# Kernel tuning notes

Measured on AMD Instinct MI355X. Metric: run time of the kernel, lower is better.

The kernel has to match this reference:

```python
import jax, jax.numpy as jnp
import numpy as np

H = 32  # hidden size


def _gru_layer(x_seq, W_ih, W_hh, b_ih, b_hh):
    """x_seq: [B, T, in] -> outputs [B, T, H], final h [B, H]. PyTorch gate order (r, z, n)."""
    B = x_seq.shape[0]
    # Precompute input projections for all timesteps: [T, B, 3H]
    xw = jnp.einsum('bti,gi->tbg', x_seq, W_ih) + b_ih
    h0 = jnp.zeros((B, H), dtype=x_seq.dtype)

    def step(h, xw_t):
        gh = h @ W_hh.T + b_hh                       # [B, 3H]
        r = jax.nn.sigmoid(xw_t[:, :H] + gh[:, :H])
        z = jax.nn.sigmoid(xw_t[:, H:2 * H] + gh[:, H:2 * H])
        n = jnp.tanh(xw_t[:, 2 * H:] + r * gh[:, 2 * H:])
        h_new = (1.0 - z) * n + z * h
        return h_new, h_new

    h_last, ys = jax.lax.scan(step, h0, xw)
    return jnp.transpose(ys, (1, 0, 2)), h_last       # [B, T, H], [B, H]


def setup_inputs() -> dict:
    key = jax.random.key(0)
    ks = jax.random.split(key, 11)
    s = 1.0 / np.sqrt(H)  # PyTorch GRU init scale
    return {
        'x': jax.random.normal(ks[0], (4096, 512, 32), dtype=jnp.float32),
        'W_ih0': jax.random.uniform(ks[1], (96, 32), jnp.float32, -s, s),
        'W_hh0': jax.random.uniform(ks[2], (96, 32), jnp.float32, -s, s),
        'b_ih0': jax.random.uniform(ks[3], (96,), jnp.float32, -s, s),
        'b_hh0': jax.random.uniform(ks[4], (96,), jnp.float32, -s, s),
        'W_ih1': jax.random.uniform(ks[5], (96, 32), jnp.float32, -s, s),
        'W_hh1': jax.random.uniform(ks[6], (96, 32), jnp.float32, -s, s),
        'b_ih1': jax.random.uniform(ks[7], (96,), jnp.float32, -s, s),
        'b_hh1': jax.random.uniform(ks[8], (96,), jnp.float32, -s, s),
        'W_proj': jax.random.uniform(ks[9], (16, 32), jnp.float32, -s, s),
        'b_proj': jax.random.uniform(ks[10], (16,), jnp.float32, -s, s),
    }


def reference(x, W_ih0, W_hh0, b_ih0, b_hh0, W_ih1, W_hh1, b_ih1, b_hh1, W_proj, b_proj):
    y0, _ = _gru_layer(x, W_ih0, W_hh0, b_ih0, b_hh0)        # layer 0 full sequence
    _, h_last = _gru_layer(y0, W_ih1, W_hh1, b_ih1, b_hh1)   # layer 1 final hidden
    # dropout is identity in eval mode
    return h_last @ W_proj.T + b_proj                        # [B, 16]
```

## Files before the change

### kernel.cpp

```cpp
#include <hip/hip_runtime.h>

using bf16x8 = __attribute__((ext_vector_type(8))) short;
using short8 = __attribute__((ext_vector_type(8))) short;
using s16x4  = __attribute__((ext_vector_type(4))) short;
using f32x4  = __attribute__((ext_vector_type(4))) float;
using u32x4  = __attribute__((ext_vector_type(4))) unsigned;
using ull    = unsigned long long;

#define T_SEQ 512
#define MFMA(A, B, C) __builtin_amdgcn_mfma_f32_16x16x32_bf16((A), (B), (C), 0, 0, 0)

#define BARRIER()                                            \
    do {                                                     \
        __builtin_amdgcn_sched_barrier(0);                   \
        asm volatile("s_waitcnt lgkmcnt(0)" ::: "memory");   \
        __builtin_amdgcn_s_barrier();                        \
        __builtin_amdgcn_sched_barrier(0);                   \
    } while (0)

static constexpr float NL2E  = -1.44269504f;
static constexpr float N2L2E = -2.88539008f;

__device__ __forceinline__ void split8_tr(f32x4 a, f32x4 b, bf16x8& hi, bf16x8& lo) {
    u32x4 ua = __builtin_bit_cast(u32x4, a);
    u32x4 ub = __builtin_bit_cast(u32x4, b);
    u32x4 m  = {0xffff0000u, 0xffff0000u, 0xffff0000u, 0xffff0000u};
    f32x4 ra = a - __builtin_bit_cast(f32x4, ua & m);
    f32x4 rb = b - __builtin_bit_cast(f32x4, ub & m);
    short8 sa  = __builtin_bit_cast(short8, a);
    short8 sb  = __builtin_bit_cast(short8, b);
    short8 sra = __builtin_bit_cast(short8, ra);
    short8 srb = __builtin_bit_cast(short8, rb);
    hi = __builtin_shufflevector(sa, sb, 1, 3, 5, 7, 9, 11, 13, 15);
    lo = __builtin_shufflevector(sra, srb, 1, 3, 5, 7, 9, 11, 13, 15);
}

__device__ __forceinline__ void split4_tr(f32x4 a, s16x4& hi, s16x4& lo) {
    u32x4 ua = __builtin_bit_cast(u32x4, a);
    u32x4 m  = {0xffff0000u, 0xffff0000u, 0xffff0000u, 0xffff0000u};
    f32x4 ra = a - __builtin_bit_cast(f32x4, ua & m);
    short8 sa  = __builtin_bit_cast(short8, a);
    short8 sra = __builtin_bit_cast(short8, ra);
    hi = __builtin_shufflevector(sa, sa, 1, 3, 5, 7);
    lo = __builtin_shufflevector(sra, sra, 1, 3, 5, 7);
}

__device__ __forceinline__ bf16x8 combine8(ull lo8, ull hi8) {
    u32x4 v = {(unsigned)lo8, (unsigned)(lo8 >> 32),
               (unsigned)hi8, (unsigned)(hi8 >> 32)};
    return __builtin_bit_cast(bf16x8, v);
}
__device__ __forceinline__ bf16x8 combine8_sel(ull own, ull other, int m) {
    return combine8(m ? other : own, m ? own : other);
}

__device__ __forceinline__ void mfma9(const bf16x8 (&WH)[3], const bf16x8 (&WL)[3],
                                      bf16x8 inh, bf16x8 inl,
                                      f32x4 c0, f32x4 c1, f32x4 c2,
                                      f32x4& a0, f32x4& a1, f32x4& a2) {
    a0 = MFMA(WH[0], inh, c0); a1 = MFMA(WH[1], inh, c1); a2 = MFMA(WH[2], inh, c2);
    a0 = MFMA(WH[0], inl, a0); a1 = MFMA(WH[1], inl, a1); a2 = MFMA(WH[2], inl, a2);
    a0 = MFMA(WL[0], inh, a0); a1 = MFMA(WL[1], inh, a1); a2 = MFMA(WL[2], inh, a2);
}

__device__ __forceinline__ void gate4(f32x4 aR, f32x4 aZ, f32x4 iN, f32x4 sN,
                                      float (&hf)[4]) {
    float er[4], ez[4];
    #pragma unroll
    for (int j = 0; j < 4; ++j) er[j] = __builtin_amdgcn_exp2f(aR[j] * NL2E);
    #pragma unroll
    for (int j = 0; j < 4; ++j) ez[j] = __builtin_amdgcn_exp2f(aZ[j] * NL2E);
    float gr[4], gz[4];
    #pragma unroll
    for (int j = 0; j < 4; ++j) gr[j] = __builtin_amdgcn_rcpf(1.f + er[j]);
    #pragma unroll
    for (int j = 0; j < 4; ++j) gz[j] = __builtin_amdgcn_rcpf(1.f + ez[j]);
    float en[4];
    #pragma unroll
    for (int j = 0; j < 4; ++j) {
        float u = fmaf(gr[j], sN[j], iN[j]);
        en[j] = __builtin_amdgcn_exp2f(fminf(u * N2L2E, 126.f));
    }
    float qn[4];
    #pragma unroll
    for (int j = 0; j < 4; ++j) qn[j] = __builtin_amdgcn_rcpf(1.f + en[j]);
    #pragma unroll
    for (int j = 0; j < 4; ++j) {
        float nn = fmaf(en[j] * qn[j], -2.f, 1.f);
        hf[j] = fmaf(gz[j], hf[j] - nn, nn);
    }
}

__global__ __launch_bounds__(256, 1)
void gru2_quad(const float* __restrict__ x,
               const float* __restrict__ W_ih0, const float* __restrict__ W_hh0,
               const float* __restrict__ b_ih0, const float* __restrict__ b_hh0,
               const float* __restrict__ W_ih1, const float* __restrict__ W_hh1,
               const float* __restrict__ b_ih1, const float* __restrict__ b_hh1,
               const float* __restrict__ W_proj, const float* __restrict__ b_proj,
               float* __restrict__ out)
{
    const int tid  = threadIdx.x;
    const int wid  = tid >> 6;
    const int L    = wid >> 1;
    const int m    = wid & 1;
    const int lane = tid & 63;
    const int r16  = lane & 15;
    const int q    = lane >> 4;
    const int b0   = blockIdx.x * 16;

    __shared__ ull pubH_[2][2][2][64];
    __shared__ ull pubL_[2][2][2][64];

    const float* Wx = L ? W_ih1 : W_ih0;
    const float* Wh = L ? W_hh1 : W_hh0;
    const float* bx = L ? b_ih1 : b_ih0;
    const float* bh = L ? b_hh1 : b_hh0;

    bf16x8 WxH[3], WxL[3], WhH[3], WhL[3];
    f32x4 bxf[3], bhf[3];
    #pragma unroll
    for (int g = 0; g < 3; ++g) {
        const int tile = 2 * g + m;
        const float* p1 = Wx + (16 * tile + r16) * 32 + 4 * q;
        split8_tr(*(const f32x4*)p1, *(const f32x4*)(p1 + 16), WxH[g], WxL[g]);
        const float* p2 = Wh + (16 * tile + r16) * 32 + 4 * q;
        split8_tr(*(const f32x4*)p2, *(const f32x4*)(p2 + 16), WhH[g], WhL[g]);
        bxf[g] = *(const f32x4*)(bx + 16 * tile + 4 * q);
        bhf[g] = *(const f32x4*)(bh + 16 * tile + 4 * q);
    }

    float hf[4] = {0.f, 0.f, 0.f, 0.f};
    ull ownH = 0, ownL = 0;
    const float* xp = x + (size_t)(b0 + r16) * (T_SEQ * 32) + 4 * q;
    f32x4 xA = {}, xB = {};
    bf16x8 xh_cur = {}, xl_cur = {};

    if (L == 0) {
        f32x4 x0A = *(const f32x4*)(xp);
        f32x4 x0B = *(const f32x4*)(xp + 16);
        xA = *(const f32x4*)(xp + 32);
        xB = *(const f32x4*)(xp + 48);
        split8_tr(x0A, x0B, xh_cur, xl_cur);
        f32x4 iR, iZ, iN;
        mfma9(WxH, WxL, xh_cur, xl_cur, bxf[0], bxf[1], bxf[2], iR, iZ, iN);
        gate4(iR + bhf[0], iZ + bhf[1], iN, bhf[2], hf);
        s16x4 hi4, lo4;
        split4_tr(f32x4{hf[0], hf[1], hf[2], hf[3]}, hi4, lo4);
        ownH = __builtin_bit_cast(ull, hi4);
        ownL = __builtin_bit_cast(ull, lo4);
        pubH_[m][0][0][lane] = ownH;
        pubL_[m][0][0][lane] = ownL;
        split8_tr(xA, xB, xh_cur, xl_cur);
        xA = *(const f32x4*)(xp + 64);
        xB = *(const f32x4*)(xp + 80);
    } else {
        pubH_[m][1][1][lane] = 0;
        pubL_[m][1][1][lane] = 0;
    }

    #pragma unroll 1
    for (int t = 1; t < T_SEQ; ++t) {
        BARRIER();
        const int pPrev = (t - 1) & 1;
        const int pCur  = t & 1;
        f32x4 iR, iZ, iN, sR, sZ, sN;
        if (L == 0) {
            ull oH = pubH_[1 - m][0][pPrev][lane];
            ull oL = pubL_[1 - m][0][pPrev][lane];
            mfma9(WxH, WxL, xh_cur, xl_cur, bxf[0], bxf[1], bxf[2], iR, iZ, iN);
            bf16x8 Sh = combine8_sel(ownH, oH, m);
            bf16x8 Sl = combine8_sel(ownL, oL, m);
            mfma9(WhH, WhL, Sh, Sl, bhf[0], bhf[1], bhf[2], sR, sZ, sN);
            split8_tr(xA, xB, xh_cur, xl_cur);
            const int tn = (t + 2 < T_SEQ) ? t + 2 : T_SEQ - 1;
            xA = *(const f32x4*)(xp + (size_t)tn * 32);
            xB = *(const f32x4*)(xp + (size_t)tn * 32 + 16);
        } else {
            ull i0H = pubH_[0][0][pPrev][lane];
            ull i1H = pubH_[1][0][pPrev][lane];
            ull i0L = pubL_[0][0][pPrev][lane];
            ull i1L = pubL_[1][0][pPrev][lane];
            ull oH  = pubH_[1 - m][1][pCur][lane];
            ull oL  = pubL_[1 - m][1][pCur][lane];
            bf16x8 inh = combine8(i0H, i1H);
            bf16x8 inl = combine8(i0L, i1L);
            mfma9(WxH, WxL, inh, inl, bxf[0], bxf[1], bxf[2], iR, iZ, iN);
            bf16x8 Sh = combine8_sel(ownH, oH, m);
            bf16x8 Sl = combine8_sel(ownL, oL, m);
            mfma9(WhH, WhL, Sh, Sl, bhf[0], bhf[1], bhf[2], sR, sZ, sN);
        }

        gate4(sR + iR, sZ + iZ, iN, sN, hf);

        s16x4 hi4, lo4;
        split4_tr(f32x4{hf[0], hf[1], hf[2], hf[3]}, hi4, lo4);
        ownH = __builtin_bit_cast(ull, hi4);
        ownL = __builtin_bit_cast(ull, lo4);
        const int pW = (L == 0) ? pCur : pPrev;
        pubH_[m][L][pW][lane] = ownH;
        pubL_[m][L][pW][lane] = ownL;
    }

    __syncthreads();
    if (L == 1) {
        bf16x8 inh = combine8(pubH_[0][0][1][lane], pubH_[1][0][1][lane]);
        bf16x8 inl = combine8(pubL_[0][0][1][lane], pubL_[1][0][1][lane]);
        bf16x8 Sh  = combine8_sel(ownH, pubH_[1 - m][1][0][lane], m);
        bf16x8 Sl  = combine8_sel(ownL, pubL_[1 - m][1][0][lane], m);
        f32x4 iR, iZ, iN, sR, sZ, sN;
        mfma9(WxH, WxL, inh, inl, bxf[0], bxf[1], bxf[2], iR, iZ, iN);
        mfma9(WhH, WhL, Sh, Sl, bhf[0], bhf[1], bhf[2], sR, sZ, sN);
        gate4(sR + iR, sZ + iZ, iN, sN, hf);
        s16x4 hi4, lo4;
        split4_tr(f32x4{hf[0], hf[1], hf[2], hf[3]}, hi4, lo4);
        pubH_[m][1][1][lane] = __builtin_bit_cast(ull, hi4);
        pubL_[m][1][1][lane] = __builtin_bit_cast(ull, lo4);
    }
    __syncthreads();

    if (wid == 2) {
        bf16x8 Hh = combine8(pubH_[0][1][1][lane], pubH_[1][1][1][lane]);
        bf16x8 Hl = combine8(pubL_[0][1][1][lane], pubL_[1][1][1][lane]);
        const float* pp = W_proj + r16 * 32 + 4 * q;
        bf16x8 Wph, Wpl;
        split8_tr(*(const f32x4*)pp, *(const f32x4*)(pp + 16), Wph, Wpl);
        f32x4 accp = *(const f32x4*)(b_proj + 4 * q);
        accp = MFMA(Wph, Hh, accp);
        accp = MFMA(Wph, Hl, accp);
        accp = MFMA(Wpl, Hh, accp);
        #pragma unroll
        for (int rg = 0; rg < 4; ++rg)
            out[(b0 + r16) * 16 + 4 * q + rg] = accp[rg];
    }
}

extern "C" void kernel_launch(void* const* d_in, const int* in_sizes, int n_in,
                              void* d_out, int out_size, void* d_ws, size_t ws_size,
                              hipStream_t stream) {
    const float* x      = (const float*)d_in[0];
    const float* W_ih0  = (const float*)d_in[1];
    const float* W_hh0  = (const float*)d_in[2];
    const float* b_ih0  = (const float*)d_in[3];
    const float* b_hh0  = (const float*)d_in[4];
    const float* W_ih1  = (const float*)d_in[5];
    const float* W_hh1  = (const float*)d_in[6];
    const float* b_ih1  = (const float*)d_in[7];
    const float* b_hh1  = (const float*)d_in[8];
    const float* W_proj = (const float*)d_in[9];
    const float* b_proj = (const float*)d_in[10];
    float* out = (float*)d_out;

    const int nb   = in_sizes[0] / (T_SEQ * 32);
    const int grid = nb / 16;

    hipLaunchKernelGGL(gru2_quad, dim3(grid), dim3(256), 0, stream,
                       x, W_ih0, W_hh0, b_ih0, b_hh0,
                       W_ih1, W_hh1, b_ih1, b_hh1, W_proj, b_proj, out);
}
```

Before: 295.6 us.

## Process two 16-row batch groups per block to interleave independent recurrences

Each block now handles 32 batch rows as two independent 16-row groups. The MFMA, gate and LDS exchange work for both groups is interleaved inside each timestep. The aim is to hide the serial latency of the recurrence behind the independent group and to halve the number of barriers per batch row. The cost is half as many blocks, which may leave CUs idle, and longer per-step critical paths.

```diff
diff --git a/kernel.cpp b/kernel.cpp
--- a/kernel.cpp
+++ b/kernel.cpp
@@ -63,42 +63,57 @@
     a0 = MFMA(WL[0], inh, a0); a1 = MFMA(WL[1], inh, a1); a2 = MFMA(WL[2], inh, a2);
 }
 
-__device__ __forceinline__ void gate4(f32x4 aR, f32x4 aZ, f32x4 iN, f32x4 sN,
-                                      float (&hf)[4]) {
-    float er[4], ez[4];
-    #pragma unroll
-    for (int j = 0; j < 4; ++j) er[j] = __builtin_amdgcn_exp2f(aR[j] * NL2E);
-    #pragma unroll
-    for (int j = 0; j < 4; ++j) ez[j] = __builtin_amdgcn_exp2f(aZ[j] * NL2E);
-    float gr[4], gz[4];
-    #pragma unroll
-    for (int j = 0; j < 4; ++j) gr[j] = __builtin_amdgcn_rcpf(1.f + er[j]);
-    #pragma unroll
-    for (int j = 0; j < 4; ++j) gz[j] = __builtin_amdgcn_rcpf(1.f + ez[j]);
-    float en[4];
-    #pragma unroll
-    for (int j = 0; j < 4; ++j) {
-        float u = fmaf(gr[j], sN[j], iN[j]);
-        en[j] = __builtin_amdgcn_exp2f(fminf(u * N2L2E, 126.f));
-    }
-    float qn[4];
-    #pragma unroll
-    for (int j = 0; j < 4; ++j) qn[j] = __builtin_amdgcn_rcpf(1.f + en[j]);
-    #pragma unroll
-    for (int j = 0; j < 4; ++j) {
-        float nn = fmaf(en[j] * qn[j], -2.f, 1.f);
-        hf[j] = fmaf(gz[j], hf[j] - nn, nn);
-    }
+__device__ __forceinline__ void gate4x2(const f32x4 (&aR)[2], const f32x4 (&aZ)[2],
+                                        const f32x4 (&iN)[2], const f32x4 (&sN)[2],
+                                        float (&hf)[2][4]) {
+    float er[2][4], ez[2][4];
+    #pragma unroll
+    for (int g = 0; g < 2; ++g)
+        #pragma unroll
+        for (int j = 0; j < 4; ++j) er[g][j] = __builtin_amdgcn_exp2f(aR[g][j] * NL2E);
+    #pragma unroll
+    for (int g = 0; g < 2; ++g)
+        #pragma unroll
+        for (int j = 0; j < 4; ++j) ez[g][j] = __builtin_amdgcn_exp2f(aZ[g][j] * NL2E);
+    float gr[2][4], gz[2][4];
+    #pragma unroll
+    for (int g = 0; g < 2; ++g)
+        #pragma unroll
+        for (int j = 0; j < 4; ++j) gr[g][j] = __builtin_amdgcn_rcpf(1.f + er[g][j]);
+    #pragma unroll
+    for (int g = 0; g < 2; ++g)
+        #pragma unroll
+        for (int j = 0; j < 4; ++j) gz[g][j] = __builtin_amdgcn_rcpf(1.f + ez[g][j]);
+    float en[2][4];
+    #pragma unroll
+    for (int g = 0; g < 2; ++g)
+        #pragma unroll
+        for (int j = 0; j < 4; ++j) {
+            float u = fmaf(gr[g][j], sN[g][j], iN[g][j]);
+            en[g][j] = __builtin_amdgcn_exp2f(fminf(u * N2L2E, 126.f));
+        }
+    float qn[2][4];
+    #pragma unroll
+    for (int g = 0; g < 2; ++g)
+        #pragma unroll
+        for (int j = 0; j < 4; ++j) qn[g][j] = __builtin_amdgcn_rcpf(1.f + en[g][j]);
+    #pragma unroll
+    for (int g = 0; g < 2; ++g)
+        #pragma unroll
+        for (int j = 0; j < 4; ++j) {
+            float nn = fmaf(en[g][j] * qn[g][j], -2.f, 1.f);
+            hf[g][j] = fmaf(gz[g][j], hf[g][j] - nn, nn);
+        }
 }
 
 __global__ __launch_bounds__(256, 1)
-void gru2_quad(const float* __restrict__ x,
-               const float* __restrict__ W_ih0, const float* __restrict__ W_hh0,
-               const float* __restrict__ b_ih0, const float* __restrict__ b_hh0,
-               const float* __restrict__ W_ih1, const float* __restrict__ W_hh1,
-               const float* __restrict__ b_ih1, const float* __restrict__ b_hh1,
-               const float* __restrict__ W_proj, const float* __restrict__ b_proj,
-               float* __restrict__ out)
+void gru2_quad2(const float* __restrict__ x,
+                const float* __restrict__ W_ih0, const float* __restrict__ W_hh0,
+                const float* __restrict__ b_ih0, const float* __restrict__ b_hh0,
+                const float* __restrict__ W_ih1, const float* __restrict__ W_hh1,
+                const float* __restrict__ b_ih1, const float* __restrict__ b_hh1,
+                const float* __restrict__ W_proj, const float* __restrict__ b_proj,
+                float* __restrict__ out)
 {
     const int tid  = threadIdx.x;
     const int wid  = tid >> 6;
@@ -107,10 +122,10 @@
     const int lane = tid & 63;
     const int r16  = lane & 15;
     const int q    = lane >> 4;
-    const int b0   = blockIdx.x * 16;
-
-    __shared__ ull pubH_[2][2][2][64];
-    __shared__ ull pubL_[2][2][2][64];
+    const int b0   = blockIdx.x * 32;
+
+    __shared__ ull pubH_[2][2][2][2][64];
+    __shared__ ull pubL_[2][2][2][2][64];
 
     const float* Wx = L ? W_ih1 : W_ih0;
     const float* Wh = L ? W_hh1 : W_hh0;
@@ -130,33 +145,55 @@
         bhf[g] = *(const f32x4*)(bh + 16 * tile + 4 * q);
     }
 
-    float hf[4] = {0.f, 0.f, 0.f, 0.f};
-    ull ownH = 0, ownL = 0;
-    const float* xp = x + (size_t)(b0 + r16) * (T_SEQ * 32) + 4 * q;
-    f32x4 xA = {}, xB = {};
-    bf16x8 xh_cur = {}, xl_cur = {};
+    float hf[2][4] = {{0.f, 0.f, 0.f, 0.f}, {0.f, 0.f, 0.f, 0.f}};
+    ull ownH[2] = {0, 0}, ownL[2] = {0, 0};
+    const float* xp[2];
+    #pragma unroll
+    for (int g = 0; g < 2; ++g)
+        xp[g] = x + (size_t)(b0 + 16 * g + r16) * (T_SEQ * 32) + 4 * q;
+    f32x4 xA[2] = {}, xB[2] = {};
+    bf16x8 xh_cur[2] = {}, xl_cur[2] = {};
 
     if (L == 0) {
-        f32x4 x0A = *(const f32x4*)(xp);
-        f32x4 x0B = *(const f32x4*)(xp + 16);
-        xA = *(const f32x4*)(xp + 32);
-        xB = *(const f32x4*)(xp + 48);
-        split8_tr(x0A, x0B, xh_cur, xl_cur);
-        f32x4 iR, iZ, iN;
-        mfma9(WxH, WxL, xh_cur, xl_cur, bxf[0], bxf[1], bxf[2], iR, iZ, iN);
-        gate4(iR + bhf[0], iZ + bhf[1], iN, bhf[2], hf);
-        s16x4 hi4, lo4;
-        split4_tr(f32x4{hf[0], hf[1], hf[2], hf[3]}, hi4, lo4);
-        ownH = __builtin_bit_cast(ull, hi4);
-        ownL = __builtin_bit_cast(ull, lo4);
-        pubH_[m][0][0][lane] = ownH;
-        pubL_[m][0][0][lane] = ownL;
-        split8_tr(xA, xB, xh_cur, xl_cur);
-        xA = *(const f32x4*)(xp + 64);
-        xB = *(const f32x4*)(xp + 80);
+        f32x4 iR[2], iZ[2], iN[2];
+        #pragma unroll
+        for (int g = 0; g < 2; ++g) {
+            f32x4 a0 = *(const f32x4*)(xp[g]);
+            f32x4 b0v = *(const f32x4*)(xp[g] + 16);
+            xA[g] = *(const f32x4*)(xp[g] + 32);
+            xB[g] = *(const f32x4*)(xp[g] + 48);
+            split8_tr(a0, b0v, xh_cur[g], xl_cur[g]);
+        }
+        #pragma unroll
+        for (int g = 0; g < 2; ++g)
+            mfma9(WxH, WxL, xh_cur[g], xl_cur[g], bxf[0], bxf[1], bxf[2],
+                  iR[g], iZ[g], iN[g]);
+        f32x4 aR[2], aZ[2], sN0[2];
+        #pragma unroll
+        for (int g = 0; g < 2; ++g) {
+            aR[g] = iR[g] + bhf[0];
+            aZ[g] = iZ[g] + bhf[1];
+            sN0[g] = bhf[2];
+        }
+        gate4x2(aR, aZ, iN, sN0, hf);
+        #pragma unroll
+        for (int g = 0; g < 2; ++g) {
+            s16x4 hi4, lo4;
+            split4_tr(f32x4{hf[g][0], hf[g][1], hf[g][2], hf[g][3]}, hi4, lo4);
+            ownH[g] = __builtin_bit_cast(ull, hi4);
+            ownL[g] = __builtin_bit_cast(ull, lo4);
+            pubH_[g][m][0][0][lane] = ownH[g];
+            pubL_[g][m][0][0][lane] = ownL[g];
+            split8_tr(xA[g], xB[g], xh_cur[g], xl_cur[g]);
+            xA[g] = *(const f32x4*)(xp[g] + 64);
+            xB[g] = *(const f32x4*)(xp[g] + 80);
+        }
     } else {
-        pubH_[m][1][1][lane] = 0;
-        pubL_[m][1][1][lane] = 0;
+        #pragma unroll
+        for (int g = 0; g < 2; ++g) {
+            pubH_[g][m][1][1][lane] = 0;
+            pubL_[g][m][1][1][lane] = 0;
+        }
     }
 
     #pragma unroll 1
@@ -164,64 +201,112 @@
         BARRIER();
         const int pPrev = (t - 1) & 1;
         const int pCur  = t & 1;
-        f32x4 iR, iZ, iN, sR, sZ, sN;
+        f32x4 iR[2], iZ[2], iN[2], sR[2], sZ[2], sN[2];
         if (L == 0) {
-            ull oH = pubH_[1 - m][0][pPrev][lane];
-            ull oL = pubL_[1 - m][0][pPrev][lane];
-            mfma9(WxH, WxL, xh_cur, xl_cur, bxf[0], bxf[1], bxf[2], iR, iZ, iN);
-            bf16x8 Sh = combine8_sel(ownH, oH, m);
-            bf16x8 Sl = combine8_sel(ownL, oL, m);
-            mfma9(WhH, WhL, Sh, Sl, bhf[0], bhf[1], bhf[2], sR, sZ, sN);
-            split8_tr(xA, xB, xh_cur, xl_cur);
-            const int tn = (t + 2 < T_SEQ) ? t + 2 : T_SEQ - 1;
-            xA = *(const f32x4*)(xp + (size_t)tn * 32);
-            xB = *(const f32x4*)(xp + (size_t)tn * 32 + 16);
+            ull oH[2], oL[2];
+            #pragma unroll
+            for (int g = 0; g < 2; ++g) {
+                oH[g] = pubH_[g][1 - m][0][pPrev][lane];
+                oL[g] = pubL_[g][1 - m][0][pPrev][lane];
+            }
+            #pragma unroll
+            for (int g = 0; g < 2; ++g)
+                mfma9(WxH, WxL, xh_cur[g], xl_cur[g], bxf[0], bxf[1], bxf[2],
+                      iR[g], iZ[g], iN[g]);
+            #pragma unroll
+            for (int g = 0; g < 2; ++g) {
+                bf16x8 Sh = combine8_sel(ownH[g], oH[g], m);
+                bf16x8 Sl = combine8_sel(ownL[g], oL[g], m);
+                mfma9(WhH, WhL, Sh, Sl, bhf[0], bhf[1], bhf[2],
+                      sR[g], sZ[g], sN[g]);
+            }
+            #pragma unroll
+            for (int g = 0; g < 2; ++g) {
+                split8_tr(xA[g], xB[g], xh_cur[g], xl_cur[g]);
+                const int tn = (t + 2 < T_SEQ) ? t + 2 : T_SEQ - 1;
+                xA[g] = *(const f32x4*)(xp[g] + (size_t)tn * 32);
+                xB[g] = *(const f32x4*)(xp[g] + (size_t)tn * 32 + 16);
+            }
         } else {
-            ull i0H = pubH_[0][0][pPrev][lane];
-            ull i1H = pubH_[1][0][pPrev][lane];
-            ull i0L = pubL_[0][0][pPrev][lane];
-            ull i1L = pubL_[1][0][pPrev][lane];
-            ull oH  = pubH_[1 - m][1][pCur][lane];
-            ull oL  = pubL_[1 - m][1][pCur][lane];
-            bf16x8 inh = combine8(i0H, i1H);
-            bf16x8 inl = combine8(i0L, i1L);
-            mfma9(WxH, WxL, inh, inl, bxf[0], bxf[1], bxf[2], iR, iZ, iN);
-            bf16x8 Sh = combine8_sel(ownH, oH, m);
-            bf16x8 Sl = combine8_sel(ownL, oL, m);
-            mfma9(WhH, WhL, Sh, Sl, bhf[0], bhf[1], bhf[2], sR, sZ, sN);
-        }
-
-        gate4(sR + iR, sZ + iZ, iN, sN, hf);
-
-        s16x4 hi4, lo4;
-        split4_tr(f32x4{hf[0], hf[1], hf[2], hf[3]}, hi4, lo4);
-        ownH = __builtin_bit_cast(ull, hi4);
-        ownL = __builtin_bit_cast(ull, lo4);
+            ull i0H[2], i1H[2], i0L[2], i1L[2], oH[2], oL[2];
+            #pragma unroll
+            for (int g = 0; g < 2; ++g) {
+                i0H[g] = pubH_[g][0][0][pPrev][lane];
+                i1H[g] = pubH_[g][1][0][pPrev][lane];
+                i0L[g] = pubL_[g][0][0][pPrev][lane];
+                i1L[g] = pubL_[g][1][0][pPrev][lane];
+                oH[g]  = pubH_[g][1 - m][1][pCur][lane];
+                oL[g]  = pubL_[g][1 - m][1][pCur][lane];
+            }
+            #pragma unroll
+            for (int g = 0; g < 2; ++g) {
+                bf16x8 inh = combine8(i0H[g], i1H[g]);
+                bf16x8 inl = combine8(i0L[g], i1L[g]);
+                mfma9(WxH, WxL, inh, inl, bxf[0], bxf[1], bxf[2],
+                      iR[g], iZ[g], iN[g]);
+            }
+            #pragma unroll
+            for (int g = 0; g < 2; ++g) {
+                bf16x8 Sh = combine8_sel(ownH[g], oH[g], m);
+                bf16x8 Sl = combine8_sel(ownL[g], oL[g], m);
+                mfma9(WhH, WhL, Sh, Sl, bhf[0], bhf[1], bhf[2],
+                      sR[g], sZ[g], sN[g]);
+            }
+        }
+
+        f32x4 aR[2], aZ[2];
+        #pragma unroll
+        for (int g = 0; g < 2; ++g) {
+            aR[g] = sR[g] + iR[g];
+            aZ[g] = sZ[g] + iZ[g];
+        }
+        gate4x2(aR, aZ, iN, sN, hf);
+
         const int pW = (L == 0) ? pCur : pPrev;
-        pubH_[m][L][pW][lane] = ownH;
-        pubL_[m][L][pW][lane] = ownL;
+        #pragma unroll
+        for (int g = 0; g < 2; ++g) {
+            s16x4 hi4, lo4;
+            split4_tr(f32x4{hf[g][0], hf[g][1], hf[g][2], hf[g][3]}, hi4, lo4);
+            ownH[g] = __builtin_bit_cast(ull, hi4);
+            ownL[g] = __builtin_bit_cast(ull, lo4);
+            pubH_[g][m][L][pW][lane] = ownH[g];
+            pubL_[g][m][L][pW][lane] = ownL[g];
+        }
     }
 
     __syncthreads();
     if (L == 1) {
-        bf16x8 inh = combine8(pubH_[0][0][1][lane], pubH_[1][0][1][lane]);
-        bf16x8 inl = combine8(pubL_[0][0][1][lane], pubL_[1][0][1][lane]);
-        bf16x8 Sh  = combine8_sel(ownH, pubH_[1 - m][1][0][lane], m);
-        bf16x8 Sl  = combine8_sel(ownL, pubL_[1 - m][1][0][lane], m);
-        f32x4 iR, iZ, iN, sR, sZ, sN;
-        mfma9(WxH, WxL, inh, inl, bxf[0], bxf[1], bxf[2], iR, iZ, iN);
-        mfma9(WhH, WhL, Sh, Sl, bhf[0], bhf[1], bhf[2], sR, sZ, sN);
-        gate4(sR + iR, sZ + iZ, iN, sN, hf);
-        s16x4 hi4, lo4;
-        split4_tr(f32x4{hf[0], hf[1], hf[2], hf[3]}, hi4, lo4);
-        pubH_[m][1][1][lane] = __builtin_bit_cast(ull, hi4);
-        pubL_[m][1][1][lane] = __builtin_bit_cast(ull, lo4);
+        f32x4 iR[2], iZ[2], iN[2], sR[2], sZ[2], sN[2];
+        #pragma unroll
+        for (int g = 0; g < 2; ++g) {
+            bf16x8 inh = combine8(pubH_[g][0][0][1][lane], pubH_[g][1][0][1][lane]);
+            bf16x8 inl = combine8(pubL_[g][0][0][1][lane], pubL_[g][1][0][1][lane]);
+            mfma9(WxH, WxL, inh, inl, bxf[0], bxf[1], bxf[2], iR[g], iZ[g], iN[g]);
+            bf16x8 Sh = combine8_sel(ownH[g], pubH_[g][1 - m][1][0][lane], m);
+            bf16x8 Sl = combine8_sel(ownL[g], pubL_[g][1 - m][1][0][lane], m);
+            mfma9(WhH, WhL, Sh, Sl, bhf[0], bhf[1], bhf[2], sR[g], sZ[g], sN[g]);
+        }
+        f32x4 aR[2], aZ[2];
+        #pragma unroll
+        for (int g = 0; g < 2; ++g) {
+            aR[g] = sR[g] + iR[g];
+            aZ[g] = sZ[g] + iZ[g];
+        }
+        gate4x2(aR, aZ, iN, sN, hf);
+        #pragma unroll
+        for (int g = 0; g < 2; ++g) {
+            s16x4 hi4, lo4;
+            split4_tr(f32x4{hf[g][0], hf[g][1], hf[g][2], hf[g][3]}, hi4, lo4);
+            pubH_[g][m][1][1][lane] = __builtin_bit_cast(ull, hi4);
+            pubL_[g][m][1][1][lane] = __builtin_bit_cast(ull, lo4);
+        }
     }
     __syncthreads();
 
-    if (wid == 2) {
-        bf16x8 Hh = combine8(pubH_[0][1][1][lane], pubH_[1][1][1][lane]);
-        bf16x8 Hl = combine8(pubL_[0][1][1][lane], pubL_[1][1][1][lane]);
+    if (wid >= 2) {
+        const int g = m;
+        bf16x8 Hh = combine8(pubH_[g][0][1][1][lane], pubH_[g][1][1][1][lane]);
+        bf16x8 Hl = combine8(pubL_[g][0][1][1][lane], pubL_[g][1][1][1][lane]);
         const float* pp = W_proj + r16 * 32 + 4 * q;
         bf16x8 Wph, Wpl;
         split8_tr(*(const f32x4*)pp, *(const f32x4*)(pp + 16), Wph, Wpl);
@@ -231,7 +316,7 @@
         accp = MFMA(Wpl, Hh, accp);
         #pragma unroll
         for (int rg = 0; rg < 4; ++rg)
-            out[(b0 + r16) * 16 + 4 * q + rg] = accp[rg];
+            out[(b0 + 16 * g + r16) * 16 + 4 * q + rg] = accp[rg];
     }
 }
 
@@ -252,9 +337,9 @@
     float* out = (float*)d_out;
 
     const int nb   = in_sizes[0] / (T_SEQ * 32);
-    const int grid = nb / 16;
-
-    hipLaunchKernelGGL(gru2_quad, dim3(grid), dim3(256), 0, stream,
+    const int grid = nb / 32;
+
+    hipLaunchKernelGGL(gru2_quad2, dim3(grid), dim3(256), 0, stream,
                        x, W_ih0, W_hh0, b_ih0, b_hh0,
                        W_ih1, W_hh1, b_ih1, b_hh1, W_proj, b_proj, out);
 }
```

Measured after the change: 492.0 us. +66.4%, slower.

## Pack two 16-batch GRU groups into one 512-thread block

Applied to the files above, without the earlier changes.

The kernel now runs two independent groups of four waves in each block. Each group handles 16 batch rows with its own slice of the shared-memory exchange buffers, so each block covers 32 rows and the grid is halved. The aim is to put two independent recurrences on each SIMD so one group's MFMA and transcendental latency can hide behind the other's. The cost is that only half as many blocks are launched, so fewer CUs are used, and every per-step barrier now synchronises eight waves instead of four.

```diff
diff --git a/kernel.cpp b/kernel.cpp
--- a/kernel.cpp
+++ b/kernel.cpp
@@ -91,26 +91,28 @@
     }
 }
 
-__global__ __launch_bounds__(256, 1)
-void gru2_quad(const float* __restrict__ x,
-               const float* __restrict__ W_ih0, const float* __restrict__ W_hh0,
-               const float* __restrict__ b_ih0, const float* __restrict__ b_hh0,
-               const float* __restrict__ W_ih1, const float* __restrict__ W_hh1,
-               const float* __restrict__ b_ih1, const float* __restrict__ b_hh1,
-               const float* __restrict__ W_proj, const float* __restrict__ b_proj,
-               float* __restrict__ out)
+__global__ __launch_bounds__(512, 1)
+void gru2_dual4(const float* __restrict__ x,
+                const float* __restrict__ W_ih0, const float* __restrict__ W_hh0,
+                const float* __restrict__ b_ih0, const float* __restrict__ b_hh0,
+                const float* __restrict__ W_ih1, const float* __restrict__ W_hh1,
+                const float* __restrict__ b_ih1, const float* __restrict__ b_hh1,
+                const float* __restrict__ W_proj, const float* __restrict__ b_proj,
+                float* __restrict__ out)
 {
     const int tid  = threadIdx.x;
     const int wid  = tid >> 6;
-    const int L    = wid >> 1;
-    const int m    = wid & 1;
+    const int grp  = wid >> 2;
+    const int role = wid & 3;
+    const int L    = role >> 1;
+    const int m    = role & 1;
     const int lane = tid & 63;
     const int r16  = lane & 15;
     const int q    = lane >> 4;
-    const int b0   = blockIdx.x * 16;
-
-    __shared__ ull pubH_[2][2][2][64];
-    __shared__ ull pubL_[2][2][2][64];
+    const int b0   = blockIdx.x * 32 + grp * 16;
+
+    __shared__ ull pubH_[2][2][2][2][64];
+    __shared__ ull pubL_[2][2][2][2][64];
 
     const float* Wx = L ? W_ih1 : W_ih0;
     const float* Wh = L ? W_hh1 : W_hh0;
@@ -149,14 +151,14 @@
         split4_tr(f32x4{hf[0], hf[1], hf[2], hf[3]}, hi4, lo4);
         ownH = __builtin_bit_cast(ull, hi4);
         ownL = __builtin_bit_cast(ull, lo4);
-        pubH_[m][0][0][lane] = ownH;
-        pubL_[m][0][0][lane] = ownL;
+        pubH_[grp][m][0][0][lane] = ownH;
+        pubL_[grp][m][0][0][lane] = ownL;
         split8_tr(xA, xB, xh_cur, xl_cur);
         xA = *(const f32x4*)(xp + 64);
         xB = *(const f32x4*)(xp + 80);
     } else {
-        pubH_[m][1][1][lane] = 0;
-        pubL_[m][1][1][lane] = 0;
+        pubH_[grp][m][1][1][lane] = 0;
+        pubL_[grp][m][1][1][lane] = 0;
     }
 
     #pragma unroll 1
@@ -166,8 +168,8 @@
         const int pCur  = t & 1;
         f32x4 iR, iZ, iN, sR, sZ, sN;
         if (L == 0) {
-            ull oH = pubH_[1 - m][0][pPrev][lane];
-            ull oL = pubL_[1 - m][0][pPrev][lane];
+            ull oH = pubH_[grp][1 - m][0][pPrev][lane];
+            ull oL = pubL_[grp][1 - m][0][pPrev][lane];
             mfma9(WxH, WxL, xh_cur, xl_cur, bxf[0], bxf[1], bxf[2], iR, iZ, iN);
             bf16x8 Sh = combine8_sel(ownH, oH, m);
             bf16x8 Sl = combine8_sel(ownL, oL, m);
@@ -177,12 +179,12 @@
             xA = *(const f32x4*)(xp + (size_t)tn * 32);
             xB = *(const f32x4*)(xp + (size_t)tn * 32 + 16);
         } else {
-            ull i0H = pubH_[0][0][pPrev][lane];
-            ull i1H = pubH_[1][0][pPrev][lane];
-            ull i0L = pubL_[0][0][pPrev][lane];
-            ull i1L = pubL_[1][0][pPrev][lane];
-            ull oH  = pubH_[1 - m][1][pCur][lane];
-            ull oL  = pubL_[1 - m][1][pCur][lane];
+            ull i0H = pubH_[grp][0][0][pPrev][lane];
+            ull i1H = pubH_[grp][1][0][pPrev][lane];
+            ull i0L = pubL_[grp][0][0][pPrev][lane];
+            ull i1L = pubL_[grp][1][0][pPrev][lane];
+            ull oH  = pubH_[grp][1 - m][1][pCur][lane];
+            ull oL  = pubL_[grp][1 - m][1][pCur][lane];
             bf16x8 inh = combine8(i0H, i1H);
             bf16x8 inl = combine8(i0L, i1L);
             mfma9(WxH, WxL, inh, inl, bxf[0], bxf[1], bxf[2], iR, iZ, iN);
@@ -198,30 +200,30 @@
         ownH = __builtin_bit_cast(ull, hi4);
         ownL = __builtin_bit_cast(ull, lo4);
         const int pW = (L == 0) ? pCur : pPrev;
-        pubH_[m][L][pW][lane] = ownH;
-        pubL_[m][L][pW][lane] = ownL;
+        pubH_[grp][m][L][pW][lane] = ownH;
+        pubL_[grp][m][L][pW][lane] = ownL;
     }
 
     __syncthreads();
     if (L == 1) {
-        bf16x8 inh = combine8(pubH_[0][0][1][lane], pubH_[1][0][1][lane]);
-        bf16x8 inl = combine8(pubL_[0][0][1][lane], pubL_[1][0][1][lane]);
-        bf16x8 Sh  = combine8_sel(ownH, pubH_[1 - m][1][0][lane], m);
-        bf16x8 Sl  = combine8_sel(ownL, pubL_[1 - m][1][0][lane], m);
+        bf16x8 inh = combine8(pubH_[grp][0][0][1][lane], pubH_[grp][1][0][1][lane]);
+        bf16x8 inl = combine8(pubL_[grp][0][0][1][lane], pubL_[grp][1][0][1][lane]);
+        bf16x8 Sh  = combine8_sel(ownH, pubH_[grp][1 - m][1][0][lane], m);
+        bf16x8 Sl  = combine8_sel(ownL, pubL_[grp][1 - m][1][0][lane], m);
         f32x4 iR, iZ, iN, sR, sZ, sN;
         mfma9(WxH, WxL, inh, inl, bxf[0], bxf[1], bxf[2], iR, iZ, iN);
         mfma9(WhH, WhL, Sh, Sl, bhf[0], bhf[1], bhf[2], sR, sZ, sN);
         gate4(sR + iR, sZ + iZ, iN, sN, hf);
         s16x4 hi4, lo4;
         split4_tr(f32x4{hf[0], hf[1], hf[2], hf[3]}, hi4, lo4);
-        pubH_[m][1][1][lane] = __builtin_bit_cast(ull, hi4);
-        pubL_[m][1][1][lane] = __builtin_bit_cast(ull, lo4);
+        pubH_[grp][m][1][1][lane] = __builtin_bit_cast(ull, hi4);
+        pubL_[grp][m][1][1][lane] = __builtin_bit_cast(ull, lo4);
     }
     __syncthreads();
 
-    if (wid == 2) {
-        bf16x8 Hh = combine8(pubH_[0][1][1][lane], pubH_[1][1][1][lane]);
-        bf16x8 Hl = combine8(pubL_[0][1][1][lane], pubL_[1][1][1][lane]);
+    if (role == 2) {
+        bf16x8 Hh = combine8(pubH_[grp][0][1][1][lane], pubH_[grp][1][1][1][lane]);
+        bf16x8 Hl = combine8(pubL_[grp][0][1][1][lane], pubL_[grp][1][1][1][lane]);
         const float* pp = W_proj + r16 * 32 + 4 * q;
         bf16x8 Wph, Wpl;
         split8_tr(*(const f32x4*)pp, *(const f32x4*)(pp + 16), Wph, Wpl);
@@ -252,9 +254,9 @@
     float* out = (float*)d_out;
 
     const int nb   = in_sizes[0] / (T_SEQ * 32);
-    const int grid = nb / 16;
-
-    hipLaunchKernelGGL(gru2_quad, dim3(grid), dim3(256), 0, stream,
+    const int grid = nb / 32;
+
+    hipLaunchKernelGGL(gru2_dual4, dim3(grid), dim3(512), 0, stream,
                        x, W_ih0, W_hh0, b_ih0, b_hh0,
                        W_ih1, W_hh1, b_ih1, b_hh1, W_proj, b_proj, out);
 }
```

Measured after the change: 387.8 us. 31.2% more time.
